# Performance work log

Measured on AMD Instinct MI355X. Metric: run time of the kernel, lower is better.

Reference implementation:

```python
import jax, jax.numpy as jnp
import numpy as np

N_NODES = 100000
N_EDGES = 3200000
D_FEAT = 64
K_HOPS = 3


def setup_inputs() -> dict:
    key = jax.random.key(0)
    k1, k2, k3, k4 = jax.random.split(key, 4)
    x = jax.random.normal(k1, (N_NODES, D_FEAT), dtype=jnp.float32)
    edge_weight = jax.random.uniform(k2, (N_EDGES,), dtype=jnp.float32)
    src = jax.random.randint(k3, (N_EDGES,), 0, N_NODES, dtype=jnp.int32)
    dst = jax.random.randint(k4, (N_EDGES,), 0, N_NODES, dtype=jnp.int32)
    return {"x": x, "edge_weight": edge_weight, "src": src, "dst": dst}


def reference(x, edge_weight, src, dst):
    # k-hop weighted SpMM: h <- scatter_sum(h[src] * w, dst), repeated K_HOPS times.
    # Dropouts are identity in eval mode (rates set to 0.0).
    h = x
    for _ in range(K_HOPS):
        msg = h[src] * edge_weight[:, None]          # [E, d] gather-multiply
        h = jax.ops.segment_sum(msg, dst, num_segments=N_NODES)  # [N, d] scatter-sum
    return h
```

## Files before the change

### kernel.cpp

```cpp
#include <hip/hip_runtime.h>

#define D_FEAT 64
#define CHUNK 8192
#define BSHIFT 9
#define BSIZE 512

typedef unsigned int uint;
typedef unsigned short ushort;

static __device__ __forceinline__ ushort f2bf(float f) {
    uint u = __float_as_uint(f);
    uint r = (u + 0x7fffu + ((u >> 16) & 1u)) >> 16;
    return (ushort)r;
}
static __device__ __forceinline__ float bf2f(ushort b) {
    return __uint_as_float(((uint)b) << 16);
}

__global__ void bucket_hist(const int* __restrict__ dst, int* __restrict__ bcount, int n_edges) {
    __shared__ int h[256];
    h[threadIdx.x] = 0;
    __syncthreads();
    for (int e = blockIdx.x * blockDim.x + threadIdx.x; e < n_edges; e += gridDim.x * blockDim.x)
        atomicAdd(&h[dst[e] >> BSHIFT], 1);
    __syncthreads();
    int v = h[threadIdx.x];
    if (v) atomicAdd(&bcount[threadIdx.x], v);
}

__global__ void bucket_scan(const int* __restrict__ bcount, int* __restrict__ bbase,
                            int* __restrict__ bcursor) {
    __shared__ int s[256];
    int t = threadIdx.x;
    int v = bcount[t];
    s[t] = v;
    __syncthreads();
    for (int off = 1; off < 256; off <<= 1) {
        int u = (t >= off) ? s[t - off] : 0;
        __syncthreads();
        s[t] += u;
        __syncthreads();
    }
    int excl = s[t] - v;
    bbase[t] = excl;
    bcursor[t] = excl;
}

__global__ __launch_bounds__(256) void partition_kernel(
        const int* __restrict__ src, const int* __restrict__ dst,
        const float* __restrict__ w, int* __restrict__ bcursor,
        int2* __restrict__ inter, int n_edges) {
    __shared__ int hist[256];
    __shared__ int lofs[256];
    __shared__ int cur[256];
    __shared__ int gbase[256];
    __shared__ int2 buf[CHUNK];
    int t = threadIdx.x;
    int beg = blockIdx.x * CHUNK;
    int end = min(beg + CHUNK, n_edges);

    hist[t] = 0;
    __syncthreads();
    for (int i = beg + t; i < end; i += 256)
        atomicAdd(&hist[dst[i] >> BSHIFT], 1);
    __syncthreads();
    int v = hist[t];
    lofs[t] = v;
    __syncthreads();
    for (int off = 1; off < 256; off <<= 1) {
        int u = (t >= off) ? lofs[t - off] : 0;
        __syncthreads();
        lofs[t] += u;
        __syncthreads();
    }
    int excl = lofs[t] - v;
    __syncthreads();
    lofs[t] = excl;
    cur[t]  = excl;
    __syncthreads();
    for (int i = beg + t; i < end; i += 256) {
        int d = dst[i];
        int b = d >> BSHIFT;
        int p = atomicAdd(&cur[b], 1);
        buf[p] = make_int2((src[i] << BSHIFT) | (d & (BSIZE - 1)), __float_as_int(w[i]));
    }
    __syncthreads();
    if (hist[t]) gbase[t] = atomicAdd(&bcursor[t], hist[t]);
    __syncthreads();
    int wid = t >> 6, lane = t & 63;
    for (int b = wid; b < 256; b += 4) {
        int c = hist[b];
        if (!c) continue;
        int lo = lofs[b], gb = gbase[b];
        for (int k = lane; k < c; k += 64)
            inter[gb + k] = buf[lo + k];
    }
}

__global__ __launch_bounds__(512) void finalize_kernel(
        const int2* __restrict__ inter, const int* __restrict__ bbase,
        const int* __restrict__ bcount, uint* __restrict__ edges,
        int* __restrict__ row_ptr, int n_nodes, int n_edges) {
    __shared__ int hist[BSIZE];
    __shared__ int cur[BSIZE];
    int b = blockIdx.x;
    int t = threadIdx.x;
    int base = bbase[b];
    int cnt  = bcount[b];

    hist[t] = 0;
    __syncthreads();
    for (int i = t; i < cnt; i += BSIZE)
        atomicAdd(&hist[inter[base + i].x & (BSIZE - 1)], 1);
    __syncthreads();
    int v = hist[t];
    cur[t] = v;
    __syncthreads();
    for (int off = 1; off < BSIZE; off <<= 1) {
        int u = (t >= off) ? cur[t - off] : 0;
        __syncthreads();
        cur[t] += u;
        __syncthreads();
    }
    int excl = cur[t] - v;
    int node = (b << BSHIFT) + t;
    if (node < n_nodes) row_ptr[node] = base + excl;
    if (b == 0 && t == 0) row_ptr[n_nodes] = n_edges;
    __syncthreads();
    cur[t] = excl;
    __syncthreads();
    for (int i = t; i < cnt; i += BSIZE) {
        int2 r = inter[base + i];
        int dlo = r.x & (BSIZE - 1);
        int p = atomicAdd(&cur[dlo], 1);
        float wf = __int_as_float(r.y);
        uint wq = (uint)(wf * 32768.0f);
        if (wq > 32767u) wq = 32767u;
        edges[base + p] = ((uint)(r.x >> BSHIFT) << 15) | wq;
    }
}

__global__ void cvt_bf16(const float* __restrict__ in, ushort* __restrict__ out, int n4) {
    int i = blockIdx.x * blockDim.x + threadIdx.x;
    int stride = gridDim.x * blockDim.x;
    for (; i < n4; i += stride) {
        float4 v = ((const float4*)in)[i];
        ushort4 o;
        o.x = f2bf(v.x); o.y = f2bf(v.y); o.z = f2bf(v.z); o.w = f2bf(v.w);
        ((ushort4*)out)[i] = o;
    }
}

template <int DEPTH, bool OUT_BF16>
__global__ __launch_bounds__(256) void gather_hop(
        const ushort* __restrict__ h, const uint* __restrict__ edges,
        const int* __restrict__ row_ptr, void* __restrict__ out_v, int n_nodes) {
    int node = __builtin_amdgcn_readfirstlane(blockIdx.x * 4 + (threadIdx.x >> 6));
    if (node >= n_nodes) return;
    int f = threadIdx.x & 63;
    int beg = __builtin_amdgcn_readfirstlane(row_ptr[node]);
    int end = __builtin_amdgcn_readfirstlane(row_ptr[node + 1]);
    float acc = 0.0f;
    int j = beg;
    for (; j + DEPTH <= end; j += DEPTH) {
        #pragma unroll
        for (int k = 0; k < DEPTH; ++k) {
            uint ev = edges[j + k];
            float wv = (float)(ev & 32767u) * (1.0f / 32768.0f) + (1.0f / 65536.0f);
            acc += wv * bf2f(h[((size_t)(ev >> 15) << 6) + f]);
        }
    }
    for (; j < end; ++j) {
        uint ev = edges[j];
        float wv = (float)(ev & 32767u) * (1.0f / 32768.0f) + (1.0f / 65536.0f);
        acc += wv * bf2f(h[((size_t)(ev >> 15) << 6) + f]);
    }
    if (OUT_BF16) ((ushort*)out_v)[((size_t)node << 6) + f] = f2bf(acc);
    else          ((float*)out_v)[((size_t)node << 6) + f]  = acc;
}

extern "C" void kernel_launch(void* const* d_in, const int* in_sizes, int n_in,
                              void* d_out, int out_size, void* d_ws, size_t ws_size,
                              hipStream_t stream) {
    const float* x   = (const float*)d_in[0];
    const float* ew  = (const float*)d_in[1];
    const int*   src = (const int*)d_in[2];
    const int*   dst = (const int*)d_in[3];
    float* out = (float*)d_out;

    const int n_nodes = in_sizes[0] / D_FEAT;
    const int n_edges = in_sizes[1];
    const int nbuck   = (n_nodes + BSIZE - 1) >> BSHIFT;
    const int n_feat_total = n_nodes * D_FEAT;

    const size_t ed8_bytes = (size_t)n_edges * 8;
    const size_t ed4_bytes = (size_t)n_edges * 4;
    const size_t bf_bytes  = (size_t)n_feat_total * 2;

    char* ws = (char*)d_ws;
    int2*   inter  = (int2*)ws;
    ushort* x_bf   = (ushort*)ws;
    ushort* buf1   = (ushort*)(ws + bf_bytes);
    ws += (ed8_bytes > 2 * bf_bytes ? ed8_bytes : 2 * bf_bytes);
    uint* edges    = (uint*)ws;                 ws += ed4_bytes;
    int*  row_ptr  = (int*)ws;                  ws += (size_t)(n_nodes + 1) * 4;
    int*  bcount   = (int*)ws;                  ws += 256 * 4;
    int*  bbase    = (int*)ws;                  ws += 256 * 4;
    int*  bcursor  = (int*)ws;

    hipMemsetAsync(bcount, 0, 256 * 4, stream);
    bucket_hist<<<512, 256, 0, stream>>>(dst, bcount, n_edges);
    bucket_scan<<<1, 256, 0, stream>>>(bcount, bbase, bcursor);
    partition_kernel<<<(n_edges + CHUNK - 1) / CHUNK, 256, 0, stream>>>(
        src, dst, ew, bcursor, inter, n_edges);
    finalize_kernel<<<nbuck, BSIZE, 0, stream>>>(
        inter, bbase, bcount, edges, row_ptr, n_nodes, n_edges);

    cvt_bf16<<<1024, 256, 0, stream>>>(x, x_bf, n_feat_total / 4);

    const int grd = (n_nodes + 3) / 4;
    gather_hop< 8, true ><<<grd, 256, 0, stream>>>(x_bf, edges, row_ptr, buf1, n_nodes);
    gather_hop<16, true ><<<grd, 256, 0, stream>>>(buf1, edges, row_ptr, x_bf, n_nodes);
    gather_hop< 8, false><<<grd, 256, 0, stream>>>(x_bf, edges, row_ptr, out,  n_nodes);
}
```

Measured before the change: 318.2 us.

## Split gather across feature halves and process two edges per wavefront

```diff
diff --git a/kernel.cpp b/kernel.cpp
--- a/kernel.cpp
+++ b/kernel.cpp
@@ -151,32 +151,58 @@
     }
 }
 
-template <int DEPTH, bool OUT_BF16>
-__global__ __launch_bounds__(256) void gather_hop(
+static __device__ __forceinline__ float wq2f(uint ev) {
+    return (float)(ev & 32767u) * (1.0f / 32768.0f) + (1.0f / 65536.0f);
+}
+
+template <bool OUT_BF16>
+__global__ __launch_bounds__(256) void gather_half(
         const ushort* __restrict__ h, const uint* __restrict__ edges,
         const int* __restrict__ row_ptr, void* __restrict__ out_v, int n_nodes) {
-    int node = __builtin_amdgcn_readfirstlane(blockIdx.x * 4 + (threadIdx.x >> 6));
+    uint wg = blockIdx.x;
+    int fhalf = (int)((wg >> 2) & 1u);
+    int q     = (int)(wg & 3u);
+    int g     = (int)(wg >> 3);
+    int node  = __builtin_amdgcn_readfirstlane((g * 4 + q) * 4 + (int)(threadIdx.x >> 6));
     if (node >= n_nodes) return;
-    int f = threadIdx.x & 63;
+    int lane = threadIdx.x & 63;
+    int e2 = lane >> 5;
+    int c  = lane & 31;
+    int fcol = (fhalf << 5) + c;
     int beg = __builtin_amdgcn_readfirstlane(row_ptr[node]);
     int end = __builtin_amdgcn_readfirstlane(row_ptr[node + 1]);
+
     float acc = 0.0f;
     int j = beg;
-    for (; j + DEPTH <= end; j += DEPTH) {
+    if ((j & 1) && j < end) {
+        uint ev = edges[j];
+        if (!e2) acc += wq2f(ev) * bf2f(h[((size_t)(ev >> 15) << 6) + fcol]);
+        ++j;
+    }
+    for (; j + 16 <= end; j += 16) {
         #pragma unroll
-        for (int k = 0; k < DEPTH; ++k) {
-            uint ev = edges[j + k];
-            float wv = (float)(ev & 32767u) * (1.0f / 32768.0f) + (1.0f / 65536.0f);
-            acc += wv * bf2f(h[((size_t)(ev >> 15) << 6) + f]);
+        for (int k = 0; k < 8; ++k) {
+            uint2 evp = ((const uint2*)(edges + j))[k];
+            uint ev = e2 ? evp.y : evp.x;
+            acc += wq2f(ev) * bf2f(h[((size_t)(ev >> 15) << 6) + fcol]);
         }
     }
-    for (; j < end; ++j) {
+    for (; j + 2 <= end; j += 2) {
+        uint2 evp = *(const uint2*)(edges + j);
+        uint ev = e2 ? evp.y : evp.x;
+        acc += wq2f(ev) * bf2f(h[((size_t)(ev >> 15) << 6) + fcol]);
+    }
+    if (j < end) {
         uint ev = edges[j];
-        float wv = (float)(ev & 32767u) * (1.0f / 32768.0f) + (1.0f / 65536.0f);
-        acc += wv * bf2f(h[((size_t)(ev >> 15) << 6) + f]);
-    }
-    if (OUT_BF16) ((ushort*)out_v)[((size_t)node << 6) + f] = f2bf(acc);
-    else          ((float*)out_v)[((size_t)node << 6) + f]  = acc;
+        if (!e2) acc += wq2f(ev) * bf2f(h[((size_t)(ev >> 15) << 6) + fcol]);
+    }
+
+    acc += __shfl_xor(acc, 32);
+    if (e2 == 0) {
+        size_t o = ((size_t)node << 6) + fcol;
+        if (OUT_BF16) ((ushort*)out_v)[o] = f2bf(acc);
+        else          ((float*)out_v)[o]  = acc;
+    }
 }
 
 extern "C" void kernel_launch(void* const* d_in, const int* in_sizes, int n_in,
@@ -218,8 +244,8 @@
 
     cvt_bf16<<<1024, 256, 0, stream>>>(x, x_bf, n_feat_total / 4);
 
-    const int grd = (n_nodes + 3) / 4;
-    gather_hop< 8, true ><<<grd, 256, 0, stream>>>(x_bf, edges, row_ptr, buf1, n_nodes);
-    gather_hop<16, true ><<<grd, 256, 0, stream>>>(buf1, edges, row_ptr, x_bf, n_nodes);
-    gather_hop< 8, false><<<grd, 256, 0, stream>>>(x_bf, edges, row_ptr, out,  n_nodes);
-}
+    const int grd = ((n_nodes + 15) >> 4) * 8;
+    gather_half<true ><<<grd, 256, 0, stream>>>(x_bf, edges, row_ptr, buf1, n_nodes);
+    gather_half<true ><<<grd, 256, 0, stream>>>(buf1, edges, row_ptr, x_bf, n_nodes);
+    gather_half<false><<<grd, 256, 0, stream>>>(x_bf, edges, row_ptr, out,  n_nodes);
+}
```

Result: slower. 445.5 us (+40.0%).

## Process multiple nodes per wave in gather and flatten partition scatter

Applied to the files above, without the earlier changes.

```diff
diff --git a/kernel.cpp b/kernel.cpp
--- a/kernel.cpp
+++ b/kernel.cpp
@@ -1,12 +1,14 @@
 #include <hip/hip_runtime.h>
 
 #define D_FEAT 64
-#define CHUNK 8192
+#define CHUNK 4096
 #define BSHIFT 9
 #define BSIZE 512
+#define NPW 8
 
 typedef unsigned int uint;
 typedef unsigned short ushort;
+typedef unsigned char uchar;
 
 static __device__ __forceinline__ ushort f2bf(float f) {
     uint u = __float_as_uint(f);
@@ -15,6 +17,9 @@
 }
 static __device__ __forceinline__ float bf2f(ushort b) {
     return __uint_as_float(((uint)b) << 16);
+}
+static __device__ __forceinline__ float wq2f(uint ev) {
+    return (float)(ev & 32767u) * (1.0f / 32768.0f) + (1.0f / 65536.0f);
 }
 
 __global__ void bucket_hist(const int* __restrict__ dst, int* __restrict__ bcount, int n_edges) {
@@ -55,9 +60,11 @@
     __shared__ int cur[256];
     __shared__ int gbase[256];
     __shared__ int2 buf[CHUNK];
+    __shared__ uchar bb[CHUNK];
     int t = threadIdx.x;
     int beg = blockIdx.x * CHUNK;
     int end = min(beg + CHUNK, n_edges);
+    int cnt = end - beg;
 
     hist[t] = 0;
     __syncthreads();
@@ -83,17 +90,14 @@
         int b = d >> BSHIFT;
         int p = atomicAdd(&cur[b], 1);
         buf[p] = make_int2((src[i] << BSHIFT) | (d & (BSIZE - 1)), __float_as_int(w[i]));
+        bb[p] = (uchar)b;
     }
     __syncthreads();
     if (hist[t]) gbase[t] = atomicAdd(&bcursor[t], hist[t]);
     __syncthreads();
-    int wid = t >> 6, lane = t & 63;
-    for (int b = wid; b < 256; b += 4) {
-        int c = hist[b];
-        if (!c) continue;
-        int lo = lofs[b], gb = gbase[b];
-        for (int k = lane; k < c; k += 64)
-            inter[gb + k] = buf[lo + k];
+    for (int i = t; i < cnt; i += 256) {
+        int b = bb[i];
+        inter[gbase[b] + (i - lofs[b])] = buf[i];
     }
 }
 
@@ -151,32 +155,43 @@
     }
 }
 
-template <int DEPTH, bool OUT_BF16>
+template <bool OUT_BF16>
 __global__ __launch_bounds__(256) void gather_hop(
         const ushort* __restrict__ h, const uint* __restrict__ edges,
         const int* __restrict__ row_ptr, void* __restrict__ out_v, int n_nodes) {
-    int node = __builtin_amdgcn_readfirstlane(blockIdx.x * 4 + (threadIdx.x >> 6));
-    if (node >= n_nodes) return;
+    int wv = blockIdx.x * 4 + (threadIdx.x >> 6);
+    int n0 = __builtin_amdgcn_readfirstlane(wv * NPW);
+    if (n0 >= n_nodes) return;
     int f = threadIdx.x & 63;
-    int beg = __builtin_amdgcn_readfirstlane(row_ptr[node]);
-    int end = __builtin_amdgcn_readfirstlane(row_ptr[node + 1]);
-    float acc = 0.0f;
-    int j = beg;
-    for (; j + DEPTH <= end; j += DEPTH) {
-        #pragma unroll
-        for (int k = 0; k < DEPTH; ++k) {
-            uint ev = edges[j + k];
-            float wv = (float)(ev & 32767u) * (1.0f / 32768.0f) + (1.0f / 65536.0f);
-            acc += wv * bf2f(h[((size_t)(ev >> 15) << 6) + f]);
+
+    int rp[NPW + 1];
+    #pragma unroll
+    for (int i = 0; i <= NPW; ++i)
+        rp[i] = row_ptr[min(n0 + i, n_nodes)];
+
+    #pragma unroll
+    for (int ni = 0; ni < NPW; ++ni) {
+        int node = n0 + ni;
+        if (node >= n_nodes) break;
+        int beg = __builtin_amdgcn_readfirstlane(rp[ni]);
+        int end = __builtin_amdgcn_readfirstlane(rp[ni + 1]);
+        float acc = 0.0f;
+        int j = beg;
+        for (; j + 8 <= end; j += 8) {
+            #pragma unroll
+            for (int k = 0; k < 8; ++k) {
+                uint ev = edges[j + k];
+                acc += wq2f(ev) * bf2f(h[((size_t)(ev >> 15) << 6) + f]);
+            }
         }
-    }
-    for (; j < end; ++j) {
-        uint ev = edges[j];
-        float wv = (float)(ev & 32767u) * (1.0f / 32768.0f) + (1.0f / 65536.0f);
-        acc += wv * bf2f(h[((size_t)(ev >> 15) << 6) + f]);
-    }
-    if (OUT_BF16) ((ushort*)out_v)[((size_t)node << 6) + f] = f2bf(acc);
-    else          ((float*)out_v)[((size_t)node << 6) + f]  = acc;
+        for (; j < end; ++j) {
+            uint ev = edges[j];
+            acc += wq2f(ev) * bf2f(h[((size_t)(ev >> 15) << 6) + f]);
+        }
+        size_t o = ((size_t)node << 6) + f;
+        if (OUT_BF16) ((ushort*)out_v)[o] = f2bf(acc);
+        else          ((float*)out_v)[o]  = acc;
+    }
 }
 
 extern "C" void kernel_launch(void* const* d_in, const int* in_sizes, int n_in,
@@ -218,8 +233,9 @@
 
     cvt_bf16<<<1024, 256, 0, stream>>>(x, x_bf, n_feat_total / 4);
 
-    const int grd = (n_nodes + 3) / 4;
-    gather_hop< 8, true ><<<grd, 256, 0, stream>>>(x_bf, edges, row_ptr, buf1, n_nodes);
-    gather_hop<16, true ><<<grd, 256, 0, stream>>>(buf1, edges, row_ptr, x_bf, n_nodes);
-    gather_hop< 8, false><<<grd, 256, 0, stream>>>(x_bf, edges, row_ptr, out,  n_nodes);
-}
+    const int waves = (n_nodes + NPW - 1) / NPW;
+    const int grd = (waves + 3) / 4;
+    gather_hop<true ><<<grd, 256, 0, stream>>>(x_bf, edges, row_ptr, buf1, n_nodes);
+    gather_hop<true ><<<grd, 256, 0, stream>>>(buf1, edges, row_ptr, x_bf, n_nodes);
+    gather_hop<false><<<grd, 256, 0, stream>>>(x_bf, edges, row_ptr, out,  n_nodes);
+}
```

After: 315.0 us. Within noise of the previous version (-1.0%).
